# Kernel tuning notes

Measured on AMD Instinct MI355X. Metric: run time of the kernel, lower is better.

The kernel has to match this reference:

```python
import jax, jax.numpy as jnp
import numpy as np

N, E, C, H, W = 5000, 80000, 32, 8, 8


def setup_inputs() -> dict:
    key = jax.random.key(0)
    k1, k2, k3, k4, k5, k6 = jax.random.split(key, 6)
    h = jax.random.normal(k1, (N, C, H, W), dtype=jnp.float32)
    e = jax.random.uniform(k2, (E,), dtype=jnp.float32)
    src = jax.random.randint(k3, (E,), 0, N, dtype=jnp.int32)
    # ensure every node receives at least one message (avoids -inf segments),
    # matching a connected graph where update_all covers all nodes
    dst = jnp.concatenate([jnp.arange(N, dtype=jnp.int32),
                           jax.random.randint(k4, (E - N,), 0, N, dtype=jnp.int32)])
    fan_in = C * 3 * 3
    bound = float(1.0 / np.sqrt(fan_in))
    conv_w = jax.random.uniform(k5, (C, C, 3, 3), minval=-bound, maxval=bound, dtype=jnp.float32)
    conv_b = jax.random.uniform(k6, (C,), minval=-bound, maxval=bound, dtype=jnp.float32)
    return {"h": h, "e": e, "conv_w": conv_w, "conv_b": conv_b, "src": src, "dst": dst}


def reference(h, e, conv_w, conv_b, src, dst):
    # message: gather source features per edge, scale by scalar edge weight
    m = e[:, None, None, None] * h[src]                      # [E, C, H, W]
    # conv2d(dim->dim, k=3, pad=1) + exact GELU, edges as batch dim
    m = jax.lax.conv_general_dilated(
        m, conv_w, window_strides=(1, 1), padding='SAME',
        dimension_numbers=('NCHW', 'OIHW', 'NCHW'))
    m = jax.nn.gelu(m + conv_b[None, :, None, None], approximate=False)
    # reduce: ragged max over each destination node's mailbox
    out = jax.ops.segment_max(m, dst, num_segments=h.shape[0])  # [N, C, H, W]
    return out
```

## Files before the change

### kernel.cpp

```cpp
#include <hip/hip_runtime.h>
#include <math.h>

#define CCH   32
#define HWPIX 64
#define CHW   2048
#define NHALF 2500
#define HT_STRIDE 40
#define HT_NODE   2600

typedef __attribute__((ext_vector_type(8))) short bf16x8;
typedef __attribute__((ext_vector_type(4))) float f32x4;
typedef __fp16 fp16x2 __attribute__((ext_vector_type(2)));
typedef unsigned int uint_t;
typedef unsigned short ushort_t;

__device__ __forceinline__ ushort_t f2bf(float f) {
    uint_t u = __float_as_uint(f);
    u += 0x7fffu + ((u >> 16) & 1u);
    return (ushort_t)(u >> 16);
}

__device__ __forceinline__ uint_t pkh2(float a, float b) {
    fp16x2 p = __builtin_amdgcn_cvt_pkrtz(a, b);
    uint_t u;
    __builtin_memcpy(&u, &p, 4);
    return u;
}

__device__ __forceinline__ float h_lo(uint_t u) {
    ushort_t s = (ushort_t)u;
    __fp16 h;
    __builtin_memcpy(&h, &s, 2);
    return (float)h;
}
__device__ __forceinline__ float h_hi(uint_t u) { return h_lo(u >> 16); }

__device__ __forceinline__ float fgelu(float x) {
    float x2 = x * x;
    float t = x * fmaf(0.0713548162726f, x2, 1.5957691216f);
    float ez = __expf(-t);
    return x * __builtin_amdgcn_rcpf(1.0f + ez);
}


__global__ __launch_bounds__(256) void hist_prep_kernel(
    const int* __restrict__ dst, int* cnt, int ne, int nhist,
    const float* __restrict__ w, ushort_t* __restrict__ wfrag) {
    int b = blockIdx.x;
    if (b < nhist) {
        int i = b * 256 + threadIdx.x;
        if (i < ne) atomicAdd(&cnt[dst[i]], 1);
    } else {
        for (int idx = threadIdx.x; idx < 18 * 64; idx += 256) {
            int ch = idx / (9 * 64);
            int rem = idx % (9 * 64);
            int tap = rem / 64;
            int l = rem % 64;
            int co = ch * 16 + (l & 15);
            int g = l >> 4;
            for (int j = 0; j < 8; j++) {
                int ci = g * 8 + j;
                wfrag[(size_t)idx * 8 + j] = f2bf(w[(co * CCH + ci) * 9 + tap]);
            }
        }
    }
}

__global__ __launch_bounds__(256) void scan_kernel(const int* __restrict__ cnt,
                                                   int* __restrict__ offs,
                                                   int* __restrict__ cursor,
                                                   int nn) {
    __shared__ int part[256];
    int t = threadIdx.x;
    int per = (nn + 255) >> 8;
    if (per > 32) per = 32;
    int base = t * per;
    int local[32];
    int sum = 0;
    for (int i = 0; i < per; i++) {
        int idx = base + i;
        int v = (idx < nn) ? cnt[idx] : 0;
        local[i] = sum;
        sum += v;
    }
    part[t] = sum;
    __syncthreads();
    int acc = sum;
    for (int d = 1; d < 256; d <<= 1) {
        int tv = (t >= d) ? part[t - d] : 0;
        __syncthreads();
        acc += tv;
        part[t] = acc;
        __syncthreads();
    }
    int excl = acc - sum;
    for (int i = 0; i < per; i++) {
        int idx = base + i;
        if (idx < nn) {
            int o = excl + local[i];
            offs[idx] = o;
            cursor[idx] = o;
        }
    }
    if (t == 255) offs[nn] = acc;
}

__global__ __launch_bounds__(256) void conv_scatter_kernel(
    const float* __restrict__ h, const ushort_t* __restrict__ wfrag,
    ushort_t* __restrict__ convh, int nconv,
    const int* __restrict__ dst, const int* __restrict__ src,
    const float* __restrict__ e, int* cursor, int2* __restrict__ swA, int ne) {
    __shared__ ushort_t Ht[2 * HT_NODE];
    int b = blockIdx.x;
    int t = threadIdx.x;

    if (b >= nconv) {
        int i = (b - nconv) * 256 + t;
        if (i < ne) {
            int p = atomicAdd(&cursor[dst[i]], 1);
            int2 v;
            v.x = src[i];
            v.y = __float_as_int(e[i]);
            swA[p] = v;
        }
        return;
    }

    int node0 = b * 2;
    uint_t* Hd = (uint_t*)Ht;
#pragma unroll
    for (int nd = 0; nd < 2; nd++) {
        const float* hn = h + (size_t)(node0 + nd) * CHW;
#pragma unroll
        for (int it = 0; it < 4; it++) {
            int ci2 = it * 4 + (t >> 6);
            int p = t & 63;
            float a = hn[ci2 * 128 + p];
            float bb = hn[ci2 * 128 + 64 + p];
            uint_t val = (uint_t)f2bf(a) | ((uint_t)f2bf(bb) << 16);
            Hd[nd * (HT_NODE / 2) + p * (HT_STRIDE / 2) + ci2] = val;
        }
    }
    if (t < 40) Hd[0 * (HT_NODE / 2) + 64 * (HT_STRIDE / 2) + (t % 20)] = 0;
    if (t >= 40 && t < 80) Hd[1 * (HT_NODE / 2) + 64 * (HT_STRIDE / 2) + (t - 40) % 20] = 0;
    __syncthreads();

    int l = t & 63;
    int w = __builtin_amdgcn_readfirstlane(t >> 6);
    int nd = w >> 1;
    int ch = w & 1;
    int s = l & 15, g = l >> 4;
    int n = node0 + nd;

    bf16x8 A[9];
#pragma unroll
    for (int tap = 0; tap < 9; tap++)
        A[tap] = ((const bf16x8*)wfrag)[(ch * 9 + tap) * 64 + l];

    f32x4 C[4];
#pragma unroll
    for (int i = 0; i < 4; i++) C[i] = (f32x4){0.f, 0.f, 0.f, 0.f};

    const short* HtS = (const short*)(Ht + nd * HT_NODE);
#pragma unroll
    for (int tau = 0; tau < 4; tau++) {
        int p = tau * 16 + s;
        int y = p >> 3, x = p & 7;
#pragma unroll
        for (int tap = 0; tap < 9; tap++) {
            int dy = tap / 3 - 1, dx = tap % 3 - 1;
            int yy = y + dy, xx = x + dx;
            bool valid = (yy >= 0) & (yy < 8) & (xx >= 0) & (xx < 8);
            int pp = valid ? (yy * 8 + xx) : 64;
            bf16x8 B = *(const bf16x8*)&HtS[pp * HT_STRIDE + g * 8];
            C[tau] = __builtin_amdgcn_mfma_f32_16x16x32_bf16(A[tap], B, C[tau], 0, 0, 0);
        }
    }

    ushort_t* outn = convh + (size_t)n * CHW;
#pragma unroll
    for (int tau = 0; tau < 4; tau++) {
        uint2 v;
        v.x = pkh2(C[tau][0], C[tau][1]);
        v.y = pkh2(C[tau][2], C[tau][3]);
        *(uint2*)(outn + (tau * 16 + s) * 32 + ch * 16 + g * 4) = v;
    }
}

__device__ __forceinline__ void red2h(uint_t* mn, uint_t* mx, uint_t d, uint_t w2) {
    uint_t v;
    asm("v_pk_mul_f16 %0, %1, %2" : "=v"(v) : "v"(d), "v"(w2));
    asm("v_pk_min_f16 %0, %0, %1" : "+v"(*mn) : "v"(v));
    asm("v_pk_max_f16 %0, %0, %1" : "+v"(*mx) : "v"(v));
}
__device__ __forceinline__ void red8h(uint_t* mn, uint_t* mx, uint4 qv, uint_t w2) {
    red2h(&mn[0], &mx[0], qv.x, w2);
    red2h(&mn[1], &mx[1], qv.y, w2);
    red2h(&mn[2], &mx[2], qv.z, w2);
    red2h(&mn[3], &mx[3], qv.w, w2);
}

__global__ __launch_bounds__(256) void gather_max_kernel(
    const ushort_t* __restrict__ convh, const float* __restrict__ bias,
    const int* __restrict__ offs, const int2* __restrict__ swA,
    float* __restrict__ out) {
    int t = threadIdx.x;
    int l = t & 63;
    int w = t >> 6;
    int b = blockIdx.x;
    int q = b & 3;
    int half = (b >> 2) & 1;
    int n = __builtin_amdgcn_readfirstlane(half * NHALF + (b >> 3) * 4 + w);
    int beg = offs[n], end = offs[n + 1];
    int last = end - 1;

    const char* qbase = (const char*)convh + 1024 * q + 16 * l;

    uint_t mn[4], mx[4];
#pragma unroll
    for (int i = 0; i < 4; i++) { mn[i] = 0x7c007c00u; mx[i] = 0xfc00fc00u; }

    uint4 D[8];
    uint_t Wh[8];
    int2 T[8];
#pragma unroll
    for (int k = 0; k < 8; k++) {
        int idx = beg + k; idx = idx < last ? idx : last;
        int2 d = swA[idx];
        D[k] = *(const uint4*)(qbase + (size_t)d.x * 4096);
        float wf = __int_as_float(d.y);
        Wh[k] = pkh2(wf, wf);
    }
#pragma unroll
    for (int k = 0; k < 8; k++) {
        int idx = beg + 8 + k; idx = idx < last ? idx : last;
        T[k] = swA[idx];
    }

    for (int j = beg; j < end; j += 8) {
        int2 U[8];
#pragma unroll
        for (int k = 0; k < 8; k++) {
            int idx = j + 16 + k; idx = idx < last ? idx : last;
            U[k] = swA[idx];
        }
#pragma unroll
        for (int k = 0; k < 8; k++) {
            red8h(mn, mx, D[k], Wh[k]);
            D[k] = *(const uint4*)(qbase + (size_t)T[k].x * 4096);
            float wf = __int_as_float(T[k].y);
            Wh[k] = pkh2(wf, wf);
        }
#pragma unroll
        for (int k = 0; k < 8; k++) T[k] = U[k];
    }

    const float4* b4 = (const float4*)(bias + (l & 3) * 8);
    float4 bLo = b4[0], bHi = b4[1];
    float bb[8] = {bLo.x, bLo.y, bLo.z, bLo.w, bHi.x, bHi.y, bHi.z, bHi.w};
    float* op = out + (size_t)n * CHW + (size_t)(l & 3) * 512 + q * 16 + (l >> 2);
#pragma unroll
    for (int k = 0; k < 4; k++) {
        float mx0 = h_lo(mx[k]), mx1 = h_hi(mx[k]);
        float mn0 = h_lo(mn[k]), mn1 = h_hi(mn[k]);
        op[(2 * k) * 64]     = fmaxf(fgelu(mx0 + bb[2 * k]),     fgelu(mn0 + bb[2 * k]));
        op[(2 * k + 1) * 64] = fmaxf(fgelu(mx1 + bb[2 * k + 1]), fgelu(mn1 + bb[2 * k + 1]));
    }
}

extern "C" void kernel_launch(void* const* d_in, const int* in_sizes, int n_in,
                              void* d_out, int out_size, void* d_ws, size_t ws_size,
                              hipStream_t stream) {
    const float* h      = (const float*)d_in[0];
    const float* e      = (const float*)d_in[1];
    const float* conv_w = (const float*)d_in[2];
    const float* conv_b = (const float*)d_in[3];
    const int*   src    = (const int*)d_in[4];
    const int*   dst    = (const int*)d_in[5];
    int nn = in_sizes[0] / CHW;
    int ne = in_sizes[1];

    ushort_t* convh = (ushort_t*)d_ws;
    ushort_t* wfrag = convh + (size_t)nn * CHW;
    int*   cnt    = (int*)(wfrag + 18 * 64 * 8);
    int*   offs   = cnt + nn;
    int*   cursor = offs + nn + 2;
    int2*  swA    = (int2*)(cursor + nn);

    int nhist = (ne + 255) / 256;
    int nconv = nn / 2;

    (void)hipMemsetAsync(cnt, 0, (size_t)nn * sizeof(int), stream);
    hist_prep_kernel<<<nhist + 1, 256, 0, stream>>>(dst, cnt, ne, nhist,
                                                    conv_w, wfrag);
    scan_kernel<<<1, 256, 0, stream>>>(cnt, offs, cursor, nn);
    conv_scatter_kernel<<<nconv + nhist, 256, 0, stream>>>(
        h, wfrag, convh, nconv, dst, src, e, cursor, swA, ne);
    gather_max_kernel<<<nn, 256, 0, stream>>>(convh, conv_b, offs, swA,
                                              (float*)d_out);
}
```

Measured before the change: 150.3 us.

## Move histogram into conv kernel, split scatter, fold memset into prep

The zeroing of counts moves into the prep kernel, which replaces the memset. The dst histogram now runs inside the conv kernel alongside the convolution blocks, and the edge scatter becomes its own kernel after the scan. Edge records and output stores use nontemporal stores. Launch count stays the same, with the memset swapped for a tiny kernel. The scatter no longer overlaps the conv, and the histogram now hides behind the conv work instead.

```diff
diff --git a/kernel.cpp b/kernel.cpp
--- a/kernel.cpp
+++ b/kernel.cpp
@@ -13,6 +13,7 @@
 typedef __fp16 fp16x2 __attribute__((ext_vector_type(2)));
 typedef unsigned int uint_t;
 typedef unsigned short ushort_t;
+typedef unsigned long long u64_t;
 
 __device__ __forceinline__ ushort_t f2bf(float f) {
     uint_t u = __float_as_uint(f);
@@ -42,16 +43,14 @@
     return x * __builtin_amdgcn_rcpf(1.0f + ez);
 }
 
-
-__global__ __launch_bounds__(256) void hist_prep_kernel(
-    const int* __restrict__ dst, int* cnt, int ne, int nhist,
+__global__ __launch_bounds__(256) void prep_kernel(
+    int* __restrict__ cnt, int nn,
     const float* __restrict__ w, ushort_t* __restrict__ wfrag) {
-    int b = blockIdx.x;
-    if (b < nhist) {
-        int i = b * 256 + threadIdx.x;
-        if (i < ne) atomicAdd(&cnt[dst[i]], 1);
+    int t = threadIdx.x;
+    if (blockIdx.x == 0) {
+        for (int i = t; i < nn; i += 256) cnt[i] = 0;
     } else {
-        for (int idx = threadIdx.x; idx < 18 * 64; idx += 256) {
+        for (int idx = t; idx < 18 * 64; idx += 256) {
             int ch = idx / (9 * 64);
             int rem = idx % (9 * 64);
             int tap = rem / 64;
@@ -105,24 +104,17 @@
     if (t == 255) offs[nn] = acc;
 }
 
-__global__ __launch_bounds__(256) void conv_scatter_kernel(
+__global__ __launch_bounds__(256) void conv_hist_kernel(
     const float* __restrict__ h, const ushort_t* __restrict__ wfrag,
     ushort_t* __restrict__ convh, int nconv,
-    const int* __restrict__ dst, const int* __restrict__ src,
-    const float* __restrict__ e, int* cursor, int2* __restrict__ swA, int ne) {
+    const int* __restrict__ dst, int* cnt, int ne) {
     __shared__ ushort_t Ht[2 * HT_NODE];
     int b = blockIdx.x;
     int t = threadIdx.x;
 
     if (b >= nconv) {
         int i = (b - nconv) * 256 + t;
-        if (i < ne) {
-            int p = atomicAdd(&cursor[dst[i]], 1);
-            int2 v;
-            v.x = src[i];
-            v.y = __float_as_int(e[i]);
-            swA[p] = v;
-        }
+        if (i < ne) atomicAdd(&cnt[dst[i]], 1);
         return;
     }
 
@@ -184,6 +176,17 @@
         v.x = pkh2(C[tau][0], C[tau][1]);
         v.y = pkh2(C[tau][2], C[tau][3]);
         *(uint2*)(outn + (tau * 16 + s) * 32 + ch * 16 + g * 4) = v;
+    }
+}
+
+__global__ __launch_bounds__(256) void scatter_kernel(
+    const int* __restrict__ dst, const int* __restrict__ src,
+    const float* __restrict__ e, int* cursor, int2* __restrict__ swA, int ne) {
+    int i = blockIdx.x * 256 + threadIdx.x;
+    if (i < ne) {
+        int p = atomicAdd(&cursor[dst[i]], 1);
+        u64_t v = ((u64_t)(uint_t)__float_as_int(e[i]) << 32) | (uint_t)src[i];
+        __builtin_nontemporal_store(v, (u64_t*)&swA[p]);
     }
 }
 
@@ -263,8 +266,10 @@
     for (int k = 0; k < 4; k++) {
         float mx0 = h_lo(mx[k]), mx1 = h_hi(mx[k]);
         float mn0 = h_lo(mn[k]), mn1 = h_hi(mn[k]);
-        op[(2 * k) * 64]     = fmaxf(fgelu(mx0 + bb[2 * k]),     fgelu(mn0 + bb[2 * k]));
-        op[(2 * k + 1) * 64] = fmaxf(fgelu(mx1 + bb[2 * k + 1]), fgelu(mn1 + bb[2 * k + 1]));
+        float r0 = fmaxf(fgelu(mx0 + bb[2 * k]),     fgelu(mn0 + bb[2 * k]));
+        float r1 = fmaxf(fgelu(mx1 + bb[2 * k + 1]), fgelu(mn1 + bb[2 * k + 1]));
+        __builtin_nontemporal_store(r0, &op[(2 * k) * 64]);
+        __builtin_nontemporal_store(r1, &op[(2 * k + 1) * 64]);
     }
 }
 
@@ -290,12 +295,11 @@
     int nhist = (ne + 255) / 256;
     int nconv = nn / 2;
 
-    (void)hipMemsetAsync(cnt, 0, (size_t)nn * sizeof(int), stream);
-    hist_prep_kernel<<<nhist + 1, 256, 0, stream>>>(dst, cnt, ne, nhist,
-                                                    conv_w, wfrag);
+    prep_kernel<<<2, 256, 0, stream>>>(cnt, nn, conv_w, wfrag);
+    conv_hist_kernel<<<nconv + nhist, 256, 0, stream>>>(
+        h, wfrag, convh, nconv, dst, cnt, ne);
     scan_kernel<<<1, 256, 0, stream>>>(cnt, offs, cursor, nn);
-    conv_scatter_kernel<<<nconv + nhist, 256, 0, stream>>>(
-        h, wfrag, convh, nconv, dst, src, e, cursor, swA, ne);
+    scatter_kernel<<<nhist, 256, 0, stream>>>(dst, src, e, cursor, swA, ne);
     gather_max_kernel<<<nn, 256, 0, stream>>>(convh, conv_b, offs, swA,
                                               (float*)d_out);
 }
```

Result: no change. 152.6 us (+1.5%).
